# Optimization experiments

Hardware: AMD Instinct MI355X
Metric: run time of the kernel (lower is better)

The kernel has to match this reference:

```python
import jax, jax.numpy as jnp
import numpy as np

N_NODES = 50000
N_EDGES = 640000
D_IN = 128
D_OUT = 128


def setup_inputs() -> dict:
    key = jax.random.key(0)
    k1, k2, k3, k4, k5 = jax.random.split(key, 5)
    features = jax.random.normal(k1, (N_NODES, D_IN), dtype=jnp.float32)
    src = jax.random.randint(k2, (N_EDGES,), 0, N_NODES, dtype=jnp.int64)
    dst = jax.random.randint(k3, (N_EDGES,), 0, N_NODES, dtype=jnp.int64)
    W = jax.random.normal(k4, (D_IN, D_OUT), dtype=jnp.float32)
    b = jax.random.normal(k5, (1, D_OUT), dtype=jnp.float32)
    return {"features": features, "src": src, "dst": dst, "W": W, "b": b}


def reference(features, src, dst, W, b):
    # ptens.gather: sum neighbor features into each destination node
    msgs = features[src]                                  # [E, D_IN] gathered edge messages
    agg = jax.ops.segment_sum(msgs, dst, num_segments=N_NODES)  # [N, D_IN]
    # Linear: x @ W + b
    return agg @ W + b
```

## Files before the change

### kernel.cpp

```cpp
#include <hip/hip_runtime.h>

#define N_NODES 50000
#define N_EDGES 640000
#define D 128
#define NBINS 392
#define NCHUNK 96
#define EPC 6667


typedef __attribute__((ext_vector_type(8))) short short8;
typedef __attribute__((ext_vector_type(4))) float f32x4;

static __device__ inline unsigned pkbf(float lo, float hi) {
    unsigned a = __float_as_uint(lo) + 0x8000u;
    unsigned b = __float_as_uint(hi) + 0x8000u;
    return __builtin_amdgcn_perm(b, a, 0x07060302);
}
static __device__ inline unsigned short f2bf(float f) {
    return (unsigned short)((__float_as_uint(f) + 0x8000u) >> 16);
}
static __device__ inline float bflo(unsigned u) { return __uint_as_float(u << 16); }
static __device__ inline float bfhi(unsigned u) { return __uint_as_float(u & 0xFFFF0000u); }

__global__ __launch_bounds__(1024) void hist_kernel(
        const int* __restrict__ dst,
        const float* __restrict__ W,
        uint4* __restrict__ Wf,
        unsigned* __restrict__ hist) {
    __shared__ unsigned h[NBINS];
    const int t = threadIdx.x;
    const int blk = blockIdx.x;
    if (t < NBINS) h[t] = 0;

    if (blk < 2) {
        int e = blk * 1024 + t;
        int q  = e & 3;
        int n  = (e >> 2) & 15;
        int nt = (e >> 6) & 7;
        int kt = e >> 9;
        const float* p = W + (kt * 32 + q * 8) * D + nt * 16 + n;
        unsigned u[8];
        #pragma unroll
        for (int j = 0; j < 8; ++j) u[j] = __float_as_uint(p[j * D]) + 0x8000u;
        uint4 o;
        o.x = __builtin_amdgcn_perm(u[1], u[0], 0x07060302);
        o.y = __builtin_amdgcn_perm(u[3], u[2], 0x07060302);
        o.z = __builtin_amdgcn_perm(u[5], u[4], 0x07060302);
        o.w = __builtin_amdgcn_perm(u[7], u[6], 0x07060302);
        Wf[e] = o;
    }
    __syncthreads();

    const int start = blk * EPC;
    const int end = min(start + EPC, N_EDGES);
    for (int e = start + t; e < end; e += 1024)
        atomicAdd(&h[((unsigned)dst[e]) >> 7], 1u);
    __syncthreads();
    if (t < NBINS) hist[blk * NBINS + t] = h[t];
}

__global__ __launch_bounds__(512) void scan_kernel(
        const unsigned* __restrict__ hist,
        unsigned* __restrict__ base,
        unsigned* __restrict__ binbase) {
    __shared__ unsigned tot[NBINS];
    __shared__ unsigned bbs[NBINS + 1];
    const int b = threadIdx.x;
    if (b < NBINS) {
        unsigned s = 0;
        for (int k = 0; k < NCHUNK; ++k) s += hist[k * NBINS + b];
        tot[b] = s;
    }
    __syncthreads();
    if (b == 0) {
        unsigned a = 0;
        for (int i = 0; i < NBINS; ++i) { bbs[i] = a; a += tot[i]; }
        bbs[NBINS] = a;
    }
    __syncthreads();
    if (b <= NBINS) binbase[b] = bbs[b];
    if (b < NBINS) {
        unsigned run = bbs[b];
        for (int k = 0; k < NCHUNK; ++k) {
            base[k * NBINS + b] = run;
            run += hist[k * NBINS + b];
        }
    }
}

__global__ __launch_bounds__(1024) void scatter_kernel(
        const int* __restrict__ src,
        const int* __restrict__ dst,
        const unsigned* __restrict__ base,
        unsigned* __restrict__ recs) {
    __shared__ unsigned h[NBINS];
    __shared__ unsigned lb[NBINS];
    const int t = threadIdx.x;
    const int blk = blockIdx.x;
    if (t < NBINS) { h[t] = 0; lb[t] = base[blk * NBINS + t]; }
    __syncthreads();
    const int start = blk * EPC;
    const int end = min(start + EPC, N_EDGES);
    for (int e = start + t; e < end; e += 1024) {
        int d = dst[e];
        int s = src[e];
        unsigned bin = ((unsigned)d) >> 7;
        unsigned r = atomicAdd(&h[bin], 1u);
        unsigned off = lb[bin] + r;
        if (off < N_EDGES)
            recs[off] = (((unsigned)d) << 16) | (unsigned)s;
    }
}

__global__ __launch_bounds__(256) void nodesort_kernel(
        const unsigned* __restrict__ recs,
        const unsigned* __restrict__ binbase,
        unsigned* __restrict__ nodeoff,
        unsigned short* __restrict__ edst) {
    __shared__ unsigned cnt128[128];
    __shared__ unsigned ns[129];
    __shared__ unsigned tick[128];
    const int t = threadIdx.x;
    const int b = blockIdx.x;
    const unsigned s0 = binbase[b];
    const unsigned e1 = binbase[b + 1];
    if (t < 128) cnt128[t] = 0;
    __syncthreads();
    for (unsigned i = s0 + t; i < e1; i += 256)
        atomicAdd(&cnt128[(recs[i] >> 16) & 127u], 1u);
    __syncthreads();
    if (t == 0) {
        unsigned a = 0;
        for (int i = 0; i < 128; ++i) { ns[i] = a; a += cnt128[i]; }
        ns[128] = a;
    }
    __syncthreads();
    if (t < 128) {
        tick[t] = ns[t];
        nodeoff[b * 128 + t] = s0 + ns[t];
    }
    if (b == 0 && t == 128) nodeoff[NBINS * 128] = N_EDGES;
    __syncthreads();
    for (unsigned i = s0 + t; i < e1; i += 256) {
        unsigned r = recs[i];
        unsigned off = s0 + atomicAdd(&tick[(r >> 16) & 127u], 1u);
        edst[off] = (unsigned short)(r & 0xFFFFu);
    }
}

__global__ __launch_bounds__(256) void gemm_kernel(
        const uint4* __restrict__ Wf,
        const float* __restrict__ feat,
        unsigned short* __restrict__ Y) {
    const int t = threadIdx.x;
    const int tile = blockIdx.x;
    const int wave = t >> 6;
    const int lane = t & 63;
    const int n = lane & 15;
    const int q = lane >> 4;

    short8 bfrag[4][2];
    #pragma unroll
    for (int kt = 0; kt < 4; ++kt) {
        #pragma unroll
        for (int p = 0; p < 2; ++p) {
            int nt = wave * 2 + p;
            uint4 raw = Wf[(((kt * 8 + nt) * 16 + n) << 2) + q];
            bfrag[kt][p] = *(const short8*)&raw;
        }
    }

    const float* ap = feat + (size_t)(tile * 16 + n) * D + q * 8;
    f32x4 acc0 = {0.f, 0.f, 0.f, 0.f};
    f32x4 acc1 = {0.f, 0.f, 0.f, 0.f};
    #pragma unroll
    for (int kt = 0; kt < 4; ++kt) {
        float4 f0 = *(const float4*)(ap + kt * 32);
        float4 f1 = *(const float4*)(ap + kt * 32 + 4);
        int4 pa;
        pa.x = (int)pkbf(f0.x, f0.y);
        pa.y = (int)pkbf(f0.z, f0.w);
        pa.z = (int)pkbf(f1.x, f1.y);
        pa.w = (int)pkbf(f1.z, f1.w);
        short8 afrag = *(const short8*)&pa;
        acc0 = __builtin_amdgcn_mfma_f32_16x16x32_bf16(afrag, bfrag[kt][0], acc0, 0, 0, 0);
        acc1 = __builtin_amdgcn_mfma_f32_16x16x32_bf16(afrag, bfrag[kt][1], acc1, 0, 0, 0);
    }
    unsigned short* yp = Y + (size_t)(tile * 16 + q * 4) * D + n;
    #pragma unroll
    for (int i = 0; i < 4; ++i) {
        yp[(size_t)i * D + wave * 32]      = f2bf(acc0[i]);
        yp[(size_t)i * D + wave * 32 + 16] = f2bf(acc1[i]);
    }
}

__global__ __launch_bounds__(256) void gather_kernel(
        const uint4* __restrict__ Y4,
        const unsigned* __restrict__ nodeoff,
        const unsigned short* __restrict__ edst,
        const float4* __restrict__ b4,
        float* __restrict__ out) {
    int node = (blockIdx.x * 256 + threadIdx.x) >> 6;
    int lane = threadIdx.x & 63;
    if (node >= N_NODES) return;
    unsigned start = nodeoff[node];
    int cnt = (int)(nodeoff[node + 1] - start);
    const int q = lane >> 4;
    const int c = lane & 15;

    float ax[8];
    #pragma unroll
    for (int i = 0; i < 8; ++i) ax[i] = 0.f;

    for (int c0 = 0; c0 < cnt; c0 += 64) {
        int m = min(cnt - c0, 64);
        int eid = (lane < m) ? (int)edst[start + c0 + lane] : 0;
        for (int j = 0; j < m; j += 4) {
            int idx = j + q;
            int sid = __shfl(eid, idx & 63);
            uint4 v = make_uint4(0u, 0u, 0u, 0u);
            if (idx < m) v = Y4[(size_t)sid * 16 + c];
            ax[0] += bflo(v.x); ax[1] += bfhi(v.x);
            ax[2] += bflo(v.y); ax[3] += bfhi(v.y);
            ax[4] += bflo(v.z); ax[5] += bfhi(v.z);
            ax[6] += bflo(v.w); ax[7] += bfhi(v.w);
        }
    }

    #pragma unroll
    for (int i = 0; i < 8; ++i) {
        ax[i] += __shfl_xor(ax[i], 16);
        ax[i] += __shfl_xor(ax[i], 32);
    }

    if (lane < 32) {
        int q2 = lane >> 4;
        float4 bb = b4[c * 2 + q2];
        float4 o;
        o.x = ax[q2 * 4 + 0] + bb.x;
        o.y = ax[q2 * 4 + 1] + bb.y;
        o.z = ax[q2 * 4 + 2] + bb.z;
        o.w = ax[q2 * 4 + 3] + bb.w;
        *(float4*)(out + (size_t)node * D + c * 8 + q2 * 4) = o;
    }
}

extern "C" void kernel_launch(void* const* d_in, const int* in_sizes, int n_in,
                              void* d_out, int out_size, void* d_ws, size_t ws_size,
                              hipStream_t stream) {
    const float* feat = (const float*)d_in[0];
    const int*   src  = (const int*)d_in[1];
    const int*   dst  = (const int*)d_in[2];
    const float* W    = (const float*)d_in[3];
    const float* b    = (const float*)d_in[4];
    float* out = (float*)d_out;

    unsigned short* Y = (unsigned short*)d_ws;
    uint4* Wf = (uint4*)((char*)d_ws + (size_t)N_NODES * D * 2);
    unsigned* hist    = (unsigned*)((char*)Wf + 2048 * sizeof(uint4));
    unsigned* base    = hist + NCHUNK * NBINS;
    unsigned* binbase = base + NCHUNK * NBINS;
    unsigned* nodeoff = binbase + (NBINS + 1);
    unsigned* recs    = nodeoff + (NBINS * 128 + 1);
    unsigned short* edst = (unsigned short*)(recs + N_EDGES);

    hist_kernel<<<NCHUNK, 1024, 0, stream>>>(dst, W, Wf, hist);
    scan_kernel<<<1, 512, 0, stream>>>(hist, base, binbase);
    scatter_kernel<<<NCHUNK, 1024, 0, stream>>>(src, dst, base, recs);
    nodesort_kernel<<<NBINS, 256, 0, stream>>>(recs, binbase, nodeoff, edst);
    gemm_kernel<<<3125, 256, 0, stream>>>(Wf, feat, Y);
    gather_kernel<<<N_NODES * 64 / 256, 256, 0, stream>>>(
        (const uint4*)Y, nodeoff, edst, (const float4*)b, out);
}
```

Measured before the change: 157.0 us.

## Fold scan into scatter and nodesort, vectorize index loads, unroll gather

Removes the single-block scan kernel by having each scatter and nodesort block recompute the bin totals and prefix sums from the histogram with a parallel shared-memory scan. This cuts one serialized launch and its single-block serial loop. Index arrays are now read as int4 quads in hist and scatter, nodesort moves to 512 threads, and the gather loop is unrolled by 8 so two row loads are in flight at once. In exchange every block redundantly reads the whole 96x392 histogram.

```diff
diff --git a/kernel.cpp b/kernel.cpp
--- a/kernel.cpp
+++ b/kernel.cpp
@@ -5,7 +5,8 @@
 #define D 128
 #define NBINS 392
 #define NCHUNK 96
-#define EPC 6667
+#define NQUADS 160000
+#define EPC4 1667
 
 
 typedef __attribute__((ext_vector_type(8))) short short8;
@@ -23,7 +24,7 @@
 static __device__ inline float bfhi(unsigned u) { return __uint_as_float(u & 0xFFFF0000u); }
 
 __global__ __launch_bounds__(1024) void hist_kernel(
-        const int* __restrict__ dst,
+        const int4* __restrict__ dst4,
         const float* __restrict__ W,
         uint4* __restrict__ Wf,
         unsigned* __restrict__ hist) {
@@ -51,82 +52,101 @@
     }
     __syncthreads();
 
-    const int start = blk * EPC;
-    const int end = min(start + EPC, N_EDGES);
-    for (int e = start + t; e < end; e += 1024)
-        atomicAdd(&h[((unsigned)dst[e]) >> 7], 1u);
+    const int i0 = blk * EPC4;
+    const int i1 = min(i0 + EPC4, NQUADS);
+    for (int i = i0 + t; i < i1; i += 1024) {
+        int4 d = dst4[i];
+        atomicAdd(&h[((unsigned)d.x) >> 7], 1u);
+        atomicAdd(&h[((unsigned)d.y) >> 7], 1u);
+        atomicAdd(&h[((unsigned)d.z) >> 7], 1u);
+        atomicAdd(&h[((unsigned)d.w) >> 7], 1u);
+    }
     __syncthreads();
     if (t < NBINS) hist[blk * NBINS + t] = h[t];
 }
 
-__global__ __launch_bounds__(512) void scan_kernel(
+__global__ __launch_bounds__(1024) void scatter_kernel(
+        const int4* __restrict__ src4,
+        const int4* __restrict__ dst4,
         const unsigned* __restrict__ hist,
-        unsigned* __restrict__ base,
-        unsigned* __restrict__ binbase) {
-    __shared__ unsigned tot[NBINS];
-    __shared__ unsigned bbs[NBINS + 1];
-    const int b = threadIdx.x;
-    if (b < NBINS) {
-        unsigned s = 0;
-        for (int k = 0; k < NCHUNK; ++k) s += hist[k * NBINS + b];
-        tot[b] = s;
-    }
-    __syncthreads();
-    if (b == 0) {
-        unsigned a = 0;
-        for (int i = 0; i < NBINS; ++i) { bbs[i] = a; a += tot[i]; }
-        bbs[NBINS] = a;
-    }
-    __syncthreads();
-    if (b <= NBINS) binbase[b] = bbs[b];
-    if (b < NBINS) {
-        unsigned run = bbs[b];
-        for (int k = 0; k < NCHUNK; ++k) {
-            base[k * NBINS + b] = run;
-            run += hist[k * NBINS + b];
-        }
-    }
-}
-
-__global__ __launch_bounds__(1024) void scatter_kernel(
-        const int* __restrict__ src,
-        const int* __restrict__ dst,
-        const unsigned* __restrict__ base,
         unsigned* __restrict__ recs) {
+    __shared__ unsigned sc[512];
+    __shared__ unsigned lb[NBINS];
     __shared__ unsigned h[NBINS];
-    __shared__ unsigned lb[NBINS];
     const int t = threadIdx.x;
     const int blk = blockIdx.x;
-    if (t < NBINS) { h[t] = 0; lb[t] = base[blk * NBINS + t]; }
-    __syncthreads();
-    const int start = blk * EPC;
-    const int end = min(start + EPC, N_EDGES);
-    for (int e = start + t; e < end; e += 1024) {
-        int d = dst[e];
-        int s = src[e];
-        unsigned bin = ((unsigned)d) >> 7;
-        unsigned r = atomicAdd(&h[bin], 1u);
-        unsigned off = lb[bin] + r;
-        if (off < N_EDGES)
-            recs[off] = (((unsigned)d) << 16) | (unsigned)s;
-    }
-}
-
-__global__ __launch_bounds__(256) void nodesort_kernel(
+
+    unsigned pre = 0, tot = 0;
+    if (t < NBINS)
+        for (int k = 0; k < NCHUNK; ++k) {
+            unsigned v = hist[k * NBINS + t];
+            if (k < blk) pre += v;
+            tot += v;
+        }
+    if (t < 512) sc[t] = (t < NBINS) ? tot : 0;
+    __syncthreads();
+    for (int off = 1; off < 512; off <<= 1) {
+        unsigned v = 0;
+        if (t < 512) { v = sc[t]; if (t >= off) v += sc[t - off]; }
+        __syncthreads();
+        if (t < 512) sc[t] = v;
+        __syncthreads();
+    }
+    if (t < NBINS) {
+        unsigned bbs = (t == 0) ? 0u : sc[t - 1];
+        lb[t] = bbs + pre;
+        h[t] = 0;
+    }
+    __syncthreads();
+
+    const int i0 = blk * EPC4;
+    const int i1 = min(i0 + EPC4, NQUADS);
+    for (int i = i0 + t; i < i1; i += 1024) {
+        int4 s = src4[i];
+        int4 d = dst4[i];
+        #pragma unroll
+        for (int u = 0; u < 4; ++u) {
+            int dd = (u == 0) ? d.x : (u == 1) ? d.y : (u == 2) ? d.z : d.w;
+            int ss = (u == 0) ? s.x : (u == 1) ? s.y : (u == 2) ? s.z : s.w;
+            unsigned bin = ((unsigned)dd) >> 7;
+            unsigned r = atomicAdd(&h[bin], 1u);
+            unsigned off = lb[bin] + r;
+            if (off < N_EDGES)
+                recs[off] = (((unsigned)dd) << 16) | (unsigned)ss;
+        }
+    }
+}
+
+__global__ __launch_bounds__(512) void nodesort_kernel(
+        const unsigned* __restrict__ hist,
         const unsigned* __restrict__ recs,
-        const unsigned* __restrict__ binbase,
         unsigned* __restrict__ nodeoff,
         unsigned short* __restrict__ edst) {
+    __shared__ unsigned sc[512];
     __shared__ unsigned cnt128[128];
     __shared__ unsigned ns[129];
     __shared__ unsigned tick[128];
     const int t = threadIdx.x;
     const int b = blockIdx.x;
-    const unsigned s0 = binbase[b];
-    const unsigned e1 = binbase[b + 1];
+
+    unsigned tot = 0;
+    if (t < NBINS)
+        for (int k = 0; k < NCHUNK; ++k) tot += hist[k * NBINS + t];
+    sc[t] = (t < NBINS) ? tot : 0;
+    __syncthreads();
+    for (int off = 1; off < 512; off <<= 1) {
+        unsigned v = sc[t];
+        if (t >= off) v += sc[t - off];
+        __syncthreads();
+        sc[t] = v;
+        __syncthreads();
+    }
+    const unsigned s0 = (b == 0) ? 0u : sc[b - 1];
+    const unsigned e1 = sc[b];
+
     if (t < 128) cnt128[t] = 0;
     __syncthreads();
-    for (unsigned i = s0 + t; i < e1; i += 256)
+    for (unsigned i = s0 + t; i < e1; i += 512)
         atomicAdd(&cnt128[(recs[i] >> 16) & 127u], 1u);
     __syncthreads();
     if (t == 0) {
@@ -141,7 +161,7 @@
     }
     if (b == 0 && t == 128) nodeoff[NBINS * 128] = N_EDGES;
     __syncthreads();
-    for (unsigned i = s0 + t; i < e1; i += 256) {
+    for (unsigned i = s0 + t; i < e1; i += 512) {
         unsigned r = recs[i];
         unsigned off = s0 + atomicAdd(&tick[(r >> 16) & 127u], 1u);
         edst[off] = (unsigned short)(r & 0xFFFFu);
@@ -193,6 +213,14 @@
         yp[(size_t)i * D + wave * 32 + 16] = f2bf(acc1[i]);
     }
 }
+
+#define ACC8(v)                                              \
+    do {                                                     \
+        ax[0] += bflo((v).x); ax[1] += bfhi((v).x);          \
+        ax[2] += bflo((v).y); ax[3] += bfhi((v).y);          \
+        ax[4] += bflo((v).z); ax[5] += bfhi((v).z);          \
+        ax[6] += bflo((v).w); ax[7] += bfhi((v).w);          \
+    } while (0)
 
 __global__ __launch_bounds__(256) void gather_kernel(
         const uint4* __restrict__ Y4,
@@ -215,15 +243,26 @@
     for (int c0 = 0; c0 < cnt; c0 += 64) {
         int m = min(cnt - c0, 64);
         int eid = (lane < m) ? (int)edst[start + c0 + lane] : 0;
-        for (int j = 0; j < m; j += 4) {
+        int j = 0;
+        for (; j + 8 <= m; j += 8) {
+            int sA = __shfl(eid, j + q);
+            int sB = __shfl(eid, j + 4 + q);
+            uint4 vA = Y4[(size_t)sA * 16 + c];
+            uint4 vB = Y4[(size_t)sB * 16 + c];
+            ACC8(vA);
+            ACC8(vB);
+        }
+        for (; j + 4 <= m; j += 4) {
+            int s = __shfl(eid, j + q);
+            uint4 v = Y4[(size_t)s * 16 + c];
+            ACC8(v);
+        }
+        if (j < m) {
             int idx = j + q;
-            int sid = __shfl(eid, idx & 63);
+            int s = __shfl(eid, (idx < m) ? idx : 0);
             uint4 v = make_uint4(0u, 0u, 0u, 0u);
-            if (idx < m) v = Y4[(size_t)sid * 16 + c];
-            ax[0] += bflo(v.x); ax[1] += bfhi(v.x);
-            ax[2] += bflo(v.y); ax[3] += bfhi(v.y);
-            ax[4] += bflo(v.z); ax[5] += bfhi(v.z);
-            ax[6] += bflo(v.w); ax[7] += bfhi(v.w);
+            if (idx < m) v = Y4[(size_t)s * 16 + c];
+            ACC8(v);
         }
     }
 
@@ -258,16 +297,14 @@
     unsigned short* Y = (unsigned short*)d_ws;
     uint4* Wf = (uint4*)((char*)d_ws + (size_t)N_NODES * D * 2);
     unsigned* hist    = (unsigned*)((char*)Wf + 2048 * sizeof(uint4));
-    unsigned* base    = hist + NCHUNK * NBINS;
-    unsigned* binbase = base + NCHUNK * NBINS;
-    unsigned* nodeoff = binbase + (NBINS + 1);
+    unsigned* nodeoff = hist + NCHUNK * NBINS;
     unsigned* recs    = nodeoff + (NBINS * 128 + 1);
     unsigned short* edst = (unsigned short*)(recs + N_EDGES);
 
-    hist_kernel<<<NCHUNK, 1024, 0, stream>>>(dst, W, Wf, hist);
-    scan_kernel<<<1, 512, 0, stream>>>(hist, base, binbase);
-    scatter_kernel<<<NCHUNK, 1024, 0, stream>>>(src, dst, base, recs);
-    nodesort_kernel<<<NBINS, 256, 0, stream>>>(recs, binbase, nodeoff, edst);
+    hist_kernel<<<NCHUNK, 1024, 0, stream>>>((const int4*)dst, W, Wf, hist);
+    scatter_kernel<<<NCHUNK, 1024, 0, stream>>>(
+        (const int4*)src, (const int4*)dst, hist, recs);
+    nodesort_kernel<<<NBINS, 512, 0, stream>>>(hist, recs, nodeoff, edst);
     gemm_kernel<<<3125, 256, 0, stream>>>(Wf, feat, Y);
     gather_kernel<<<N_NODES * 64 / 256, 256, 0, stream>>>(
         (const uint4*)Y, nodeoff, edst, (const float4*)b, out);
```

Result: faster. 148.5 us (-5.4%).
